# Kernel optimization log

Measured on AMD Instinct MI355X. Metric: run time of the kernel, lower is better.

Reference implementation:

```python
import jax, jax.numpy as jnp
import numpy as np

N_NODES = 50000
N_EDGES = 800000
N_ENT = 500000
N_REL = 500
L = 2          # num_layers
H = 8          # head_num
D = 16         # per-head dim (hidden_dim // head_num)
HID = H * D    # 128
IN = 128       # in_ent_dim == in_rel_dim == hidden_dim
B = 64         # number of graphs in the batch
SLOPE = 0.2    # leaky-relu negative slope


def setup_inputs() -> dict:
    key = jax.random.key(0)
    ks = jax.random.split(key, 11)
    return {
        "ent_table": jax.random.normal(ks[0], (N_ENT, IN), jnp.float32) * 0.05,
        "rel_table": jax.random.normal(ks[1], (N_REL, IN), jnp.float32) * 0.05,
        "W_ent": jax.random.normal(ks[2], (L, IN, HID), jnp.float32) * 0.05,
        "W_rel": jax.random.normal(ks[3], (L, IN, HID), jnp.float32) * 0.05,
        "attn_l": jax.random.normal(ks[4], (L, H, D), jnp.float32) * 0.05,
        "attn_r": jax.random.normal(ks[5], (L, H, D), jnp.float32) * 0.05,
        "attn_e": jax.random.normal(ks[6], (L, H, D), jnp.float32) * 0.05,
        "ent_ids": jax.random.randint(ks[7], (N_NODES,), 0, N_ENT, jnp.int32),
        "rel_ids": jax.random.randint(ks[8], (N_EDGES,), 0, N_REL, jnp.int32),
        "src": jax.random.randint(ks[9], (N_EDGES,), 0, N_NODES, jnp.int32),
        "dst": jax.random.randint(ks[10], (N_EDGES,), 0, N_NODES, jnp.int32),
        # node-0 offset of each subgraph in the batched graph
        "graph_offsets": jnp.arange(B, dtype=jnp.int32) * (N_NODES // B),
    }


def _kge_layer(h, rel_f, src, dst, W_e, W_r, a_l, a_r, a_e):
    # GAT-style relation-aware message passing (KGELayer)
    feat = (h @ W_e).reshape(-1, H, D)        # [N,H,D]
    rfeat = (rel_f @ W_r).reshape(-1, H, D)   # [E,H,D]
    el = jnp.einsum('nhd,hd->nh', feat, a_l)  # src score
    er = jnp.einsum('nhd,hd->nh', feat, a_r)  # dst score
    ee = jnp.einsum('ehd,hd->eh', rfeat, a_e) # relation score
    e = jax.nn.leaky_relu(el[src] + er[dst] + ee, SLOPE)  # [E,H]
    # segment softmax over incoming edges of each dst node
    emax = jax.ops.segment_max(e, dst, num_segments=N_NODES)
    ex = jnp.exp(e - emax[dst])
    denom = jax.ops.segment_sum(ex, dst, num_segments=N_NODES)
    alpha = ex / denom[dst]                   # [E,H]
    msg = (feat[src] + rfeat) * alpha[:, :, None]  # [E,H,D]
    out = jax.ops.segment_sum(msg, dst, num_segments=N_NODES)  # [N,H,D]
    return out.reshape(-1, HID)


def reference(ent_table, rel_table, W_ent, W_rel, attn_l, attn_r, attn_e,
              ent_ids, rel_ids, src, dst, graph_offsets):
    h = ent_table[ent_ids]       # [N,IN]
    rel_f = rel_table[rel_ids]   # [E,IN]
    for l in range(L):
        h = _kge_layer(h, rel_f, src, dst, W_ent[l], W_rel[l],
                       attn_l[l], attn_r[l], attn_e[l])
    # CLS embedding: node 0 of each unbatched subgraph
    return h[graph_offsets]      # [B,HID]
```

## Files before the change

kernel.cpp:

```cpp
#include <hip/hip_runtime.h>
#include <hip/hip_bf16.h>


#define NN   50000
#define NE   800000
#define NR   500
#define HH   8
#define DD   16
#define HIDD 128
#define BB   64

#define GRIDS 1024
#define PER   784

#define MAXE2 16384
#define MAXS1 16448
#define MAXE1 262144
#define MAXS0 50000


__global__ void k_init(int* slot2, int* slot1, int* slot0, int* counters) {
    int i = blockIdx.x * blockDim.x + threadIdx.x;
    int stride = gridDim.x * blockDim.x;
    for (int n = i; n < NN; n += stride) { slot2[n] = -1; slot1[n] = -1; slot0[n] = -1; }
    if (i < 8) counters[i] = 0;
}

__global__ void k_seed(const int* goffs, int* slot2, int* slot1, int* nodesS1) {
    int i = threadIdx.x;
    if (i < BB) {
        int n = goffs[i];
        slot2[n] = i;
        slot1[n] = -2;
        nodesS1[i] = n;
    }
}

__global__ void k_scan(const int* __restrict__ src, const int* __restrict__ dst,
                       const int* __restrict__ slotHit, int* __restrict__ slotNew,
                       int* eseg, int* ecnt, int* nseg, int* ncnt) {
    __shared__ int cE, cN;
    if (threadIdx.x == 0) { cE = 0; cN = 0; }
    __syncthreads();
    int b = blockIdx.x;
    int lo = b * PER;
    int hi = lo + PER; if (hi > NE) hi = NE;
    int* es = eseg + (size_t)b * PER;
    int* ns = nseg + (size_t)b * PER;
    for (int e = lo + threadIdx.x; e < hi; e += blockDim.x) {
        int d = dst[e];
        if (slotHit[d] >= 0) {
            int pos = atomicAdd(&cE, 1);
            es[pos] = e;
            int s = src[e];
            if (atomicCAS(&slotNew[s], -1, -2) == -1) {
                int p = atomicAdd(&cN, 1);
                ns[p] = s;
            }
        }
    }
    __syncthreads();
    if (threadIdx.x == 0) { ecnt[b] = cE; ncnt[b] = cN; }
}

__device__ int block_scan_counts(const int* cnts, int nblk, int* bases, int offset) {
    __shared__ int part[256];
    __shared__ int total_sh;
    int t = threadIdx.x;
    int per = (nblk + 255) / 256;
    int s = 0;
    for (int j = 0; j < per; j++) { int i = t * per + j; if (i < nblk) s += cnts[i]; }
    part[t] = s;
    __syncthreads();
    for (int d = 1; d < 256; d <<= 1) {
        int v = (t >= d) ? part[t - d] : 0;
        __syncthreads();
        part[t] += v;
        __syncthreads();
    }
    int run = ((t == 0) ? 0 : part[t - 1]) + offset;
    for (int j = 0; j < per; j++) {
        int i = t * per + j;
        if (i < nblk) { bases[i] = run; run += cnts[i]; }
    }
    if (t == 255) total_sh = part[255];
    __syncthreads();
    return total_sh;
}

__global__ void k_prefix2(const int* ecnt2, const int* ncnt2, int* ebase2, int* nbase2,
                          int* counters, const int* nodesS1, int* slot1, int* slot0,
                          int* nodesS0) {
    int t = threadIdx.x;
    int totE = block_scan_counts(ecnt2, GRIDS, ebase2, 0);
    int totN = block_scan_counts(ncnt2, GRIDS, nbase2, BB);
    if (t == 0) {
        counters[2] = totE;
        counters[0] = BB + totN;
        counters[1] = BB + totN;
    }
    if (t < BB) {
        int n = nodesS1[t];
        slot1[n] = t;
        slot0[n] = t;
        nodesS0[t] = n;
    }
}

__global__ void k_compact2(const int* eseg2, const int* ecnt2, const int* ebase2,
                           const int* nseg2, const int* ncnt2, const int* nbase2,
                           int* e2list, int* nodesS1, int* slot1, int* slot0,
                           int* nodesS0, int* deg2) {
    int b = blockIdx.x, t = threadIdx.x;
    int ce = ecnt2[b], cn = ncnt2[b], be = ebase2[b], bn = nbase2[b];
    const int* es = eseg2 + (size_t)b * PER;
    const int* ns = nseg2 + (size_t)b * PER;
    for (int i = t; i < ce; i += blockDim.x) {
        int g = be + i; if (g < MAXE2) e2list[g] = es[i];
    }
    for (int i = t; i < cn; i += blockDim.x) {
        int idx = bn + i;
        if (idx < MAXS1) {
            int n = ns[i];
            nodesS1[idx] = n;
            slot1[n] = idx;
            slot0[n] = idx;
            nodesS0[idx] = n;
        }
    }
    if (b == 0) { for (int i = t; i < BB; i += blockDim.x) deg2[i] = 0; }
}

__global__ void k_prefix1(const int* ecnt1, const int* ncnt1, int* ebase1, int* nbase1,
                          int* counters) {
    int t = threadIdx.x;
    int s0 = counters[1];
    int totE = block_scan_counts(ecnt1, GRIDS, ebase1, 0);
    int totN = block_scan_counts(ncnt1, GRIDS, nbase1, s0);
    if (t == 0) {
        counters[3] = totE;
        counters[1] = s0 + totN;
    }
}

__global__ void k_compact1(const int* eseg1, const int* ecnt1, const int* ebase1,
                           const int* nseg1, const int* ncnt1, const int* nbase1,
                           int* e1list, int* slot0, int* nodesS0,
                           int* deg1, const int* counters) {
    int b = blockIdx.x, t = threadIdx.x;
    int ce = ecnt1[b], cn = ncnt1[b], be = ebase1[b], bn = nbase1[b];
    const int* es = eseg1 + (size_t)b * PER;
    const int* ns = nseg1 + (size_t)b * PER;
    for (int i = t; i < ce; i += blockDim.x) {
        int g = be + i; if (g < MAXE1) e1list[g] = es[i];
    }
    for (int i = t; i < cn; i += blockDim.x) {
        int idx = bn + i;
        if (idx < MAXS0) {
            int n = ns[i];
            slot0[n] = idx;
            nodesS0[idx] = n;
        }
    }
    int cnt1 = counters[0]; if (cnt1 > MAXS1) cnt1 = MAXS1;
    for (int i = b * blockDim.x + t; i < cnt1; i += gridDim.x * blockDim.x) deg1[i] = 0;
}

__global__ void k_hist(const int* e2list, const int* e1list, const int* counters,
                       const int* dst, const int* slot2, const int* slot1,
                       int* deg2, int* deg1) {
    int i = blockIdx.x * blockDim.x + threadIdx.x;
    int stride = gridDim.x * blockDim.x;
    int c2 = counters[2]; if (c2 > MAXE2) c2 = MAXE2;
    int c1 = counters[3]; if (c1 > MAXE1) c1 = MAXE1;
    for (int k = i; k < c2; k += stride) atomicAdd(&deg2[slot2[dst[e2list[k]]]], 1);
    for (int k = i; k < c1; k += stride) atomicAdd(&deg1[slot1[dst[e1list[k]]]], 1);
}

__device__ void excl_scan_glob(const int* deg, int n, int* rp) {
    __shared__ int part[256];
    int t = threadIdx.x;
    int per = (n + 255) / 256;
    int s = 0;
    for (int j = 0; j < per; j++) { int i = t * per + j; if (i < n) s += deg[i]; }
    part[t] = s;
    __syncthreads();
    for (int d = 1; d < 256; d <<= 1) {
        int v = (t >= d) ? part[t - d] : 0;
        __syncthreads();
        part[t] += v;
        __syncthreads();
    }
    int run = (t == 0) ? 0 : part[t - 1];
    for (int j = 0; j < per; j++) {
        int i = t * per + j;
        if (i < n) { rp[i] = run; run += deg[i]; }
    }
    if (t == 255) rp[n] = part[255];
    __syncthreads();
}

__global__ void k_rowptr(const int* deg2, const int* deg1, const int* counters,
                         int* rp2, int* rp1, int* cur2, int* cur1) {
    int t = threadIdx.x;
    int cnt1 = counters[0]; if (cnt1 > MAXS1) cnt1 = MAXS1;
    excl_scan_glob(deg2, BB, rp2);
    excl_scan_glob(deg1, cnt1, rp1);
    for (int i = t; i < BB; i += blockDim.x) cur2[i] = rp2[i];
    for (int i = t; i < cnt1; i += blockDim.x) cur1[i] = rp1[i];
}

__global__ void k_scatter(const int* e2list, const int* e1list, const int* counters,
                          const int* dst, const int* slot2, const int* slot1,
                          int* cur2, int* cur1, int* csr2, int* csr1) {
    int i = blockIdx.x * blockDim.x + threadIdx.x;
    int stride = gridDim.x * blockDim.x;
    int c2 = counters[2]; if (c2 > MAXE2) c2 = MAXE2;
    int c1 = counters[3]; if (c1 > MAXE1) c1 = MAXE1;
    for (int k = i; k < c2; k += stride) {
        int e = e2list[k];
        int pos = atomicAdd(&cur2[slot2[dst[e]]], 1);
        if (pos < MAXE2) csr2[pos] = e;
    }
    for (int k = i; k < c1; k += stride) {
        int e = e1list[k];
        int pos = atomicAdd(&cur1[slot1[dst[e]]], 1);
        if (pos < MAXE1) csr1[pos] = e;
    }
}

#define FT 8
__global__ void k_relfeat0(const float* rel_table, const float* __restrict__ W_rel,
                           const float* attn_e, float* rproj, float* ee,
                           const int* nodesS0, const int* counters, const int* ent_ids,
                           const float* __restrict__ ent_table,
                           const float* __restrict__ W_ent,
                           const float* __restrict__ attn_l,
                           const float* __restrict__ attn_r,
                           float* feat0, float* el0, float* er0) {
    __shared__ float rows[FT][HIDD];
    int t = threadIdx.x;
    if (blockIdx.x < 2 * NR) {
        int l = blockIdx.x / NR, r = blockIdx.x % NR;
        rows[0][t] = rel_table[r * HIDD + t];
        __syncthreads();
        const float* W = W_rel + l * HIDD * HIDD;
        float acc = 0.f;
        for (int j = 0; j < HIDD; j++) acc += rows[0][j] * W[j * HIDD + t];
        rproj[(l * NR + r) * HIDD + t] = acc;
        rows[1][t] = acc;
        __syncthreads();
        if (t < HH) {
            float s = 0.f;
            for (int d = 0; d < DD; d++)
                s += rows[1][t * DD + d] * attn_e[(l * HH + t) * DD + d];
            ee[(l * NR + r) * HH + t] = s;
        }
        return;
    }
    int cnt = counters[1]; if (cnt > MAXS0) cnt = MAXS0;
    int tile0 = blockIdx.x - 2 * NR;
    int tstride = gridDim.x - 2 * NR;
    int nTiles = (cnt + FT - 1) / FT;
    for (int tile = tile0; tile < nTiles; tile += tstride) {
        int k0 = tile * FT;
        #pragma unroll
        for (int m = 0; m < FT; m++) {
            int k = k0 + m;
            int n = nodesS0[k < cnt ? k : 0];
            rows[m][t] = ent_table[(long)ent_ids[n] * HIDD + t];
        }
        __syncthreads();
        float acc[FT];
        #pragma unroll
        for (int m = 0; m < FT; m++) acc[m] = 0.f;
        for (int j = 0; j < HIDD; j++) {
            float w = W_ent[j * HIDD + t];
            #pragma unroll
            for (int m = 0; m < FT; m++) acc[m] += rows[m][j] * w;
        }
        __syncthreads();
        #pragma unroll
        for (int m = 0; m < FT; m++) {
            int k = k0 + m;
            if (k < cnt) feat0[k * HIDD + t] = acc[m];
            rows[m][t] = acc[m];
        }
        __syncthreads();
        {
            int m = t >> 4, idx = t & 15, h = idx >> 1, isR = idx & 1;
            int k = k0 + m;
            if (k < cnt) {
                const float* av = (isR ? attn_r : attn_l) + h * DD;
                float s = 0.f;
                for (int d = 0; d < DD; d++) s += rows[m][h * DD + d] * av[d];
                if (isR) er0[k * HH + h] = s; else el0[k * HH + h] = s;
            }
        }
        __syncthreads();
    }
}

__global__ void k_layer1(const int* counters, const int* rp1, const int* csr1,
                         const int* src, const int* rel_ids, const int* slot0,
                         const float* __restrict__ el0, const float* __restrict__ er0,
                         const float* __restrict__ ee0,
                         const float* __restrict__ feat0, const float* __restrict__ rproj0,
                         const float* __restrict__ W_ent1,
                         const float* attn_l1, const float* attn_r1,
                         float* feat1, float* el1, float* er1) {
    int cnt1 = counters[0]; if (cnt1 > MAXS1) cnt1 = MAXS1;
    int t = threadIdx.x;
    int h = t >> 4;
    __shared__ float row[HIDD];
    __shared__ float f2[HIDD];
    for (int k = blockIdx.x; k < cnt1; k += gridDim.x) {
        int lo = rp1[k], hi = rp1[k + 1];
        float er_k = er0[k * HH + h];
        float acc = 0.f, sumex = 0.f;
        for (int i = lo; i < hi; i++) {
            int e = csr1[i];
            int ks = slot0[src[e]];
            int rid = rel_ids[e];
            float sc = el0[ks * HH + h] + er_k + ee0[rid * HH + h];
            sc = sc >= 0.f ? sc : 0.2f * sc;
            float ex = __expf(sc);
            sumex += ex;
            acc += ex * (feat0[ks * HIDD + t] + rproj0[rid * HIDD + t]);
        }
        row[t] = (hi > lo) ? acc / sumex : 0.f;
        __syncthreads();
        float f = 0.f;
        for (int j = 0; j < HIDD; j++) f += row[j] * W_ent1[j * HIDD + t];
        feat1[k * HIDD + t] = f;
        f2[t] = f;
        __syncthreads();
        if (t < HH) {
            float s = 0.f;
            for (int d = 0; d < DD; d++) s += f2[t * DD + d] * attn_l1[t * DD + d];
            el1[k * HH + t] = s;
        } else if (t < 2 * HH) {
            int hh = t - HH;
            float s = 0.f;
            for (int d = 0; d < DD; d++) s += f2[hh * DD + d] * attn_r1[hh * DD + d];
            er1[k * HH + hh] = s;
        }
        __syncthreads();
    }
}

__global__ void k_layer2(const int* rp2, const int* csr2,
                         const int* src, const int* rel_ids, const int* slot1,
                         const float* __restrict__ el1, const float* __restrict__ er1,
                         const float* __restrict__ ee1,
                         const float* __restrict__ feat1, const float* __restrict__ rproj1,
                         float* out) {
    int g = blockIdx.x;
    int t = threadIdx.x;
    int h = t >> 4;
    int lo = rp2[g], hi = rp2[g + 1];
    float er_g = er1[g * HH + h];
    float acc = 0.f, sumex = 0.f;
    for (int i = lo; i < hi; i++) {
        int e = csr2[i];
        int ks = slot1[src[e]];
        int rid = rel_ids[e];
        float sc = el1[ks * HH + h] + er_g + ee1[rid * HH + h];
        sc = sc >= 0.f ? sc : 0.2f * sc;
        float ex = __expf(sc);
        sumex += ex;
        acc += ex * (feat1[ks * HIDD + t] + rproj1[rid * HIDD + t]);
    }
    out[g * HIDD + t] = (hi > lo) ? acc / sumex : 0.f;
}

extern "C" void kernel_launch(void* const* d_in, const int* in_sizes, int n_in,
                              void* d_out, int out_size, void* d_ws, size_t ws_size,
                              hipStream_t stream) {
    const float* ent_table = (const float*)d_in[0];
    const float* rel_table = (const float*)d_in[1];
    const float* W_ent     = (const float*)d_in[2];
    const float* W_rel     = (const float*)d_in[3];
    const float* attn_l    = (const float*)d_in[4];
    const float* attn_r    = (const float*)d_in[5];
    const float* attn_e    = (const float*)d_in[6];
    const int*   ent_ids   = (const int*)d_in[7];
    const int*   rel_ids   = (const int*)d_in[8];
    const int*   src       = (const int*)d_in[9];
    const int*   dst       = (const int*)d_in[10];
    const int*   goffs     = (const int*)d_in[11];
    float*       out       = (float*)d_out;

    char* p = (char*)d_ws;
    auto alloc = [&](size_t nbytes) {
        void* q = (void*)p;
        p += (nbytes + 255) & ~(size_t)255;
        return q;
    };
    float* rproj   = (float*)alloc((size_t)2 * NR * HIDD * 4);
    float* ee      = (float*)alloc((size_t)2 * NR * HH * 4);
    int*   slot2   = (int*)alloc((size_t)NN * 4);
    int*   slot1   = (int*)alloc((size_t)NN * 4);
    int*   slot0   = (int*)alloc((size_t)NN * 4);
    int*   nodesS1 = (int*)alloc((size_t)MAXS1 * 4);
    int*   nodesS0 = (int*)alloc((size_t)MAXS0 * 4);
    int*   e2list  = (int*)alloc((size_t)MAXE2 * 4);
    int*   e1list  = (int*)alloc((size_t)MAXE1 * 4);
    int*   counters= (int*)alloc(8 * 4);
    int*   eseg2   = (int*)alloc((size_t)GRIDS * PER * 4);
    int*   nseg2   = (int*)alloc((size_t)GRIDS * PER * 4);
    int*   eseg1   = (int*)alloc((size_t)GRIDS * PER * 4);
    int*   nseg1   = (int*)alloc((size_t)GRIDS * PER * 4);
    int*   ecnt2   = (int*)alloc((size_t)GRIDS * 4);
    int*   ncnt2   = (int*)alloc((size_t)GRIDS * 4);
    int*   ecnt1   = (int*)alloc((size_t)GRIDS * 4);
    int*   ncnt1   = (int*)alloc((size_t)GRIDS * 4);
    int*   ebase2  = (int*)alloc((size_t)GRIDS * 4);
    int*   nbase2  = (int*)alloc((size_t)GRIDS * 4);
    int*   ebase1  = (int*)alloc((size_t)GRIDS * 4);
    int*   nbase1  = (int*)alloc((size_t)GRIDS * 4);
    int*   deg2    = (int*)alloc((size_t)BB * 4);
    int*   rp2     = (int*)alloc((size_t)(BB + 1) * 4);
    int*   cur2    = (int*)alloc((size_t)BB * 4);
    int*   deg1    = (int*)alloc((size_t)MAXS1 * 4);
    int*   rp1     = (int*)alloc((size_t)(MAXS1 + 1) * 4);
    int*   cur1    = (int*)alloc((size_t)MAXS1 * 4);
    int*   csr2    = (int*)alloc((size_t)MAXE2 * 4);
    int*   csr1    = (int*)alloc((size_t)MAXE1 * 4);
    float* feat0   = (float*)alloc((size_t)MAXS0 * HIDD * 4);
    float* el0     = (float*)alloc((size_t)MAXS0 * HH * 4);
    float* er0     = (float*)alloc((size_t)MAXS0 * HH * 4);
    float* feat1   = (float*)alloc((size_t)MAXS1 * HIDD * 4);
    float* el1     = (float*)alloc((size_t)MAXS1 * HH * 4);
    float* er1     = (float*)alloc((size_t)MAXS1 * HH * 4);

    const float* rproj0 = rproj;
    const float* rproj1 = rproj + (size_t)NR * HIDD;
    const float* ee0 = ee;
    const float* ee1 = ee + (size_t)NR * HH;
    const float* W_ent0 = W_ent;
    const float* W_ent1 = W_ent + HIDD * HIDD;
    const float* attn_l0 = attn_l, *attn_l1 = attn_l + HH * DD;
    const float* attn_r0 = attn_r, *attn_r1 = attn_r + HH * DD;

    hipLaunchKernelGGL(k_init, dim3(256), dim3(256), 0, stream,
                       slot2, slot1, slot0, counters);
    hipLaunchKernelGGL(k_seed, dim3(1), dim3(64), 0, stream,
                       goffs, slot2, slot1, nodesS1);
    hipLaunchKernelGGL(k_scan, dim3(GRIDS), dim3(256), 0, stream,
                       src, dst, slot2, slot1, eseg2, ecnt2, nseg2, ncnt2);
    hipLaunchKernelGGL(k_prefix2, dim3(1), dim3(256), 0, stream,
                       ecnt2, ncnt2, ebase2, nbase2, counters,
                       nodesS1, slot1, slot0, nodesS0);
    hipLaunchKernelGGL(k_compact2, dim3(GRIDS), dim3(256), 0, stream,
                       eseg2, ecnt2, ebase2, nseg2, ncnt2, nbase2,
                       e2list, nodesS1, slot1, slot0, nodesS0, deg2);
    hipLaunchKernelGGL(k_scan, dim3(GRIDS), dim3(256), 0, stream,
                       src, dst, slot1, slot0, eseg1, ecnt1, nseg1, ncnt1);
    hipLaunchKernelGGL(k_prefix1, dim3(1), dim3(256), 0, stream,
                       ecnt1, ncnt1, ebase1, nbase1, counters);
    hipLaunchKernelGGL(k_compact1, dim3(GRIDS), dim3(256), 0, stream,
                       eseg1, ecnt1, ebase1, nseg1, ncnt1, nbase1,
                       e1list, slot0, nodesS0, deg1, counters);
    hipLaunchKernelGGL(k_hist, dim3(256), dim3(256), 0, stream,
                       e2list, e1list, counters, dst, slot2, slot1, deg2, deg1);
    hipLaunchKernelGGL(k_rowptr, dim3(1), dim3(256), 0, stream,
                       deg2, deg1, counters, rp2, rp1, cur2, cur1);
    hipLaunchKernelGGL(k_scatter, dim3(256), dim3(256), 0, stream,
                       e2list, e1list, counters, dst, slot2, slot1,
                       cur2, cur1, csr2, csr1);
    hipLaunchKernelGGL(k_relfeat0, dim3(2 * NR + 1024), dim3(HIDD), 0, stream,
                       rel_table, W_rel, attn_e, rproj, ee,
                       nodesS0, counters, ent_ids, ent_table, W_ent0,
                       attn_l0, attn_r0, feat0, el0, er0);
    hipLaunchKernelGGL(k_layer1, dim3(2048), dim3(HIDD), 0, stream,
                       counters, rp1, csr1, src, rel_ids, slot0,
                       el0, er0, ee0, feat0, rproj0, W_ent1,
                       attn_l1, attn_r1, feat1, el1, er1);
    hipLaunchKernelGGL(k_layer2, dim3(BB), dim3(HIDD), 0, stream,
                       rp2, csr2, src, rel_ids, slot1,
                       el1, er1, ee1, feat1, rproj1, out);
}
```

Measured before the change: 436.3 us.

## Fuse all pipeline stages into one cooperative persistent kernel with grid syncs

Measured after the change: 795.3 us. 82.3% more time.

```diff
diff --git a/kernel.cpp b/kernel.cpp
--- a/kernel.cpp
+++ b/kernel.cpp
@@ -1,5 +1,7 @@
 #include <hip/hip_runtime.h>
-#include <hip/hip_bf16.h>
+#include <hip/hip_cooperative_groups.h>
+
+namespace cg = cooperative_groups;
 
 
 #define NN   50000
@@ -10,8 +12,9 @@
 #define HIDD 128
 #define BB   64
 
-#define GRIDS 1024
-#define PER   784
+#define NBLK 256
+#define TPB  256
+#define PER  3128
 
 #define MAXE2 16384
 #define MAXS1 16448
@@ -19,53 +22,19 @@
 #define MAXS0 50000
 
 
-__global__ void k_init(int* slot2, int* slot1, int* slot0, int* counters) {
-    int i = blockIdx.x * blockDim.x + threadIdx.x;
-    int stride = gridDim.x * blockDim.x;
-    for (int n = i; n < NN; n += stride) { slot2[n] = -1; slot1[n] = -1; slot0[n] = -1; }
-    if (i < 8) counters[i] = 0;
-}
-
-__global__ void k_seed(const int* goffs, int* slot2, int* slot1, int* nodesS1) {
-    int i = threadIdx.x;
-    if (i < BB) {
-        int n = goffs[i];
-        slot2[n] = i;
-        slot1[n] = -2;
-        nodesS1[i] = n;
-    }
-}
-
-__global__ void k_scan(const int* __restrict__ src, const int* __restrict__ dst,
-                       const int* __restrict__ slotHit, int* __restrict__ slotNew,
-                       int* eseg, int* ecnt, int* nseg, int* ncnt) {
-    __shared__ int cE, cN;
-    if (threadIdx.x == 0) { cE = 0; cN = 0; }
-    __syncthreads();
-    int b = blockIdx.x;
-    int lo = b * PER;
-    int hi = lo + PER; if (hi > NE) hi = NE;
-    int* es = eseg + (size_t)b * PER;
-    int* ns = nseg + (size_t)b * PER;
-    for (int e = lo + threadIdx.x; e < hi; e += blockDim.x) {
-        int d = dst[e];
-        if (slotHit[d] >= 0) {
-            int pos = atomicAdd(&cE, 1);
-            es[pos] = e;
-            int s = src[e];
-            if (atomicCAS(&slotNew[s], -1, -2) == -1) {
-                int p = atomicAdd(&cN, 1);
-                ns[p] = s;
-            }
-        }
-    }
-    __syncthreads();
-    if (threadIdx.x == 0) { ecnt[b] = cE; ncnt[b] = cN; }
-}
-
-__device__ int block_scan_counts(const int* cnts, int nblk, int* bases, int offset) {
-    __shared__ int part[256];
-    __shared__ int total_sh;
+struct KParams {
+    const float *ent_table, *rel_table, *W_ent, *W_rel, *attn_l, *attn_r, *attn_e;
+    const int *ent_ids, *rel_ids, *src, *dst, *goffs;
+    float* out;
+    float *rproj, *ee;
+    int *slot2, *slot1, *slot0, *nodesS1, *nodesS0, *e2list, *e1list, *counters;
+    int *eseg, *nseg, *ecnt, *ncnt, *ebase, *nbase;
+    int *deg2, *rp2, *cur2, *deg1, *rp1, *cur1, *csr2, *csr1;
+    float *feat0, *el0, *er0, *feat1, *el1, *er1;
+};
+
+__device__ int block_scan_counts(const int* cnts, int nblk, int* bases, int offset,
+                                 int* part) {
     int t = threadIdx.x;
     int per = (nblk + 255) / 256;
     int s = 0;
@@ -83,102 +52,12 @@
         int i = t * per + j;
         if (i < nblk) { bases[i] = run; run += cnts[i]; }
     }
-    if (t == 255) total_sh = part[255];
+    int tot = part[255];
     __syncthreads();
-    return total_sh;
+    return tot;
 }
 
-__global__ void k_prefix2(const int* ecnt2, const int* ncnt2, int* ebase2, int* nbase2,
-                          int* counters, const int* nodesS1, int* slot1, int* slot0,
-                          int* nodesS0) {
-    int t = threadIdx.x;
-    int totE = block_scan_counts(ecnt2, GRIDS, ebase2, 0);
-    int totN = block_scan_counts(ncnt2, GRIDS, nbase2, BB);
-    if (t == 0) {
-        counters[2] = totE;
-        counters[0] = BB + totN;
-        counters[1] = BB + totN;
-    }
-    if (t < BB) {
-        int n = nodesS1[t];
-        slot1[n] = t;
-        slot0[n] = t;
-        nodesS0[t] = n;
-    }
-}
-
-__global__ void k_compact2(const int* eseg2, const int* ecnt2, const int* ebase2,
-                           const int* nseg2, const int* ncnt2, const int* nbase2,
-                           int* e2list, int* nodesS1, int* slot1, int* slot0,
-                           int* nodesS0, int* deg2) {
-    int b = blockIdx.x, t = threadIdx.x;
-    int ce = ecnt2[b], cn = ncnt2[b], be = ebase2[b], bn = nbase2[b];
-    const int* es = eseg2 + (size_t)b * PER;
-    const int* ns = nseg2 + (size_t)b * PER;
-    for (int i = t; i < ce; i += blockDim.x) {
-        int g = be + i; if (g < MAXE2) e2list[g] = es[i];
-    }
-    for (int i = t; i < cn; i += blockDim.x) {
-        int idx = bn + i;
-        if (idx < MAXS1) {
-            int n = ns[i];
-            nodesS1[idx] = n;
-            slot1[n] = idx;
-            slot0[n] = idx;
-            nodesS0[idx] = n;
-        }
-    }
-    if (b == 0) { for (int i = t; i < BB; i += blockDim.x) deg2[i] = 0; }
-}
-
-__global__ void k_prefix1(const int* ecnt1, const int* ncnt1, int* ebase1, int* nbase1,
-                          int* counters) {
-    int t = threadIdx.x;
-    int s0 = counters[1];
-    int totE = block_scan_counts(ecnt1, GRIDS, ebase1, 0);
-    int totN = block_scan_counts(ncnt1, GRIDS, nbase1, s0);
-    if (t == 0) {
-        counters[3] = totE;
-        counters[1] = s0 + totN;
-    }
-}
-
-__global__ void k_compact1(const int* eseg1, const int* ecnt1, const int* ebase1,
-                           const int* nseg1, const int* ncnt1, const int* nbase1,
-                           int* e1list, int* slot0, int* nodesS0,
-                           int* deg1, const int* counters) {
-    int b = blockIdx.x, t = threadIdx.x;
-    int ce = ecnt1[b], cn = ncnt1[b], be = ebase1[b], bn = nbase1[b];
-    const int* es = eseg1 + (size_t)b * PER;
-    const int* ns = nseg1 + (size_t)b * PER;
-    for (int i = t; i < ce; i += blockDim.x) {
-        int g = be + i; if (g < MAXE1) e1list[g] = es[i];
-    }
-    for (int i = t; i < cn; i += blockDim.x) {
-        int idx = bn + i;
-        if (idx < MAXS0) {
-            int n = ns[i];
-            slot0[n] = idx;
-            nodesS0[idx] = n;
-        }
-    }
-    int cnt1 = counters[0]; if (cnt1 > MAXS1) cnt1 = MAXS1;
-    for (int i = b * blockDim.x + t; i < cnt1; i += gridDim.x * blockDim.x) deg1[i] = 0;
-}
-
-__global__ void k_hist(const int* e2list, const int* e1list, const int* counters,
-                       const int* dst, const int* slot2, const int* slot1,
-                       int* deg2, int* deg1) {
-    int i = blockIdx.x * blockDim.x + threadIdx.x;
-    int stride = gridDim.x * blockDim.x;
-    int c2 = counters[2]; if (c2 > MAXE2) c2 = MAXE2;
-    int c1 = counters[3]; if (c1 > MAXE1) c1 = MAXE1;
-    for (int k = i; k < c2; k += stride) atomicAdd(&deg2[slot2[dst[e2list[k]]]], 1);
-    for (int k = i; k < c1; k += stride) atomicAdd(&deg1[slot1[dst[e1list[k]]]], 1);
-}
-
-__device__ void excl_scan_glob(const int* deg, int n, int* rp) {
-    __shared__ int part[256];
+__device__ void excl_scan_glob(const int* deg, int n, int* rp, int* part) {
     int t = threadIdx.x;
     int per = (n + 255) / 256;
     int s = 0;
@@ -200,196 +79,343 @@
     __syncthreads();
 }
 
-__global__ void k_rowptr(const int* deg2, const int* deg1, const int* counters,
-                         int* rp2, int* rp1, int* cur2, int* cur1) {
-    int t = threadIdx.x;
-    int cnt1 = counters[0]; if (cnt1 > MAXS1) cnt1 = MAXS1;
-    excl_scan_glob(deg2, BB, rp2);
-    excl_scan_glob(deg1, cnt1, rp1);
-    for (int i = t; i < BB; i += blockDim.x) cur2[i] = rp2[i];
-    for (int i = t; i < cnt1; i += blockDim.x) cur1[i] = rp1[i];
-}
-
-__global__ void k_scatter(const int* e2list, const int* e1list, const int* counters,
-                          const int* dst, const int* slot2, const int* slot1,
-                          int* cur2, int* cur1, int* csr2, int* csr1) {
-    int i = blockIdx.x * blockDim.x + threadIdx.x;
-    int stride = gridDim.x * blockDim.x;
-    int c2 = counters[2]; if (c2 > MAXE2) c2 = MAXE2;
-    int c1 = counters[3]; if (c1 > MAXE1) c1 = MAXE1;
-    for (int k = i; k < c2; k += stride) {
-        int e = e2list[k];
-        int pos = atomicAdd(&cur2[slot2[dst[e]]], 1);
-        if (pos < MAXE2) csr2[pos] = e;
-    }
-    for (int k = i; k < c1; k += stride) {
-        int e = e1list[k];
-        int pos = atomicAdd(&cur1[slot1[dst[e]]], 1);
-        if (pos < MAXE1) csr1[pos] = e;
-    }
-}
-
-#define FT 8
-__global__ void k_relfeat0(const float* rel_table, const float* __restrict__ W_rel,
-                           const float* attn_e, float* rproj, float* ee,
-                           const int* nodesS0, const int* counters, const int* ent_ids,
-                           const float* __restrict__ ent_table,
-                           const float* __restrict__ W_ent,
-                           const float* __restrict__ attn_l,
-                           const float* __restrict__ attn_r,
-                           float* feat0, float* el0, float* er0) {
-    __shared__ float rows[FT][HIDD];
-    int t = threadIdx.x;
-    if (blockIdx.x < 2 * NR) {
-        int l = blockIdx.x / NR, r = blockIdx.x % NR;
-        rows[0][t] = rel_table[r * HIDD + t];
-        __syncthreads();
-        const float* W = W_rel + l * HIDD * HIDD;
-        float acc = 0.f;
-        for (int j = 0; j < HIDD; j++) acc += rows[0][j] * W[j * HIDD + t];
-        rproj[(l * NR + r) * HIDD + t] = acc;
-        rows[1][t] = acc;
-        __syncthreads();
-        if (t < HH) {
-            float s = 0.f;
-            for (int d = 0; d < DD; d++)
-                s += rows[1][t * DD + d] * attn_e[(l * HH + t) * DD + d];
-            ee[(l * NR + r) * HH + t] = s;
-        }
-        return;
-    }
-    int cnt = counters[1]; if (cnt > MAXS0) cnt = MAXS0;
-    int tile0 = blockIdx.x - 2 * NR;
-    int tstride = gridDim.x - 2 * NR;
-    int nTiles = (cnt + FT - 1) / FT;
-    for (int tile = tile0; tile < nTiles; tile += tstride) {
-        int k0 = tile * FT;
-        #pragma unroll
-        for (int m = 0; m < FT; m++) {
-            int k = k0 + m;
-            int n = nodesS0[k < cnt ? k : 0];
-            rows[m][t] = ent_table[(long)ent_ids[n] * HIDD + t];
-        }
-        __syncthreads();
-        float acc[FT];
-        #pragma unroll
-        for (int m = 0; m < FT; m++) acc[m] = 0.f;
-        for (int j = 0; j < HIDD; j++) {
-            float w = W_ent[j * HIDD + t];
+__global__ void __launch_bounds__(TPB, 1) k_all(KParams P) {
+    cg::grid_group grid = cg::this_grid();
+    const int b = blockIdx.x, t = threadIdx.x;
+    const int gtid = b * TPB + t, gstride = NBLK * TPB;
+
+    __shared__ int sh_cE, sh_cN;
+    __shared__ int sh_part[256];
+    __shared__ float sh_rows[2][8][HIDD];
+
+    const float* ee0 = P.ee;
+    const float* ee1 = P.ee + NR * HH;
+    const float* rproj0 = P.rproj;
+    const float* rproj1 = P.rproj + (size_t)NR * HIDD;
+    const float* W_ent1 = P.W_ent + HIDD * HIDD;
+    const float* attn_l1 = P.attn_l + HH * DD;
+    const float* attn_r1 = P.attn_r + HH * DD;
+
+    auto scan = [&](const int* slotHit, int* slotNew) {
+        if (t == 0) { sh_cE = 0; sh_cN = 0; }
+        __syncthreads();
+        int lo = b * PER;
+        int hi = lo + PER; if (hi > NE) hi = NE;
+        int* es = P.eseg + (size_t)b * PER;
+        int* ns = P.nseg + (size_t)b * PER;
+        const int4* dst4 = (const int4*)(P.dst + lo);
+        int n4 = (hi - lo) >> 2;
+        for (int q = t; q < n4; q += TPB) {
+            int4 d4 = dst4[q];
+            int eb = lo + q * 4;
             #pragma unroll
-            for (int m = 0; m < FT; m++) acc[m] += rows[m][j] * w;
-        }
-        __syncthreads();
-        #pragma unroll
-        for (int m = 0; m < FT; m++) {
-            int k = k0 + m;
-            if (k < cnt) feat0[k * HIDD + t] = acc[m];
-            rows[m][t] = acc[m];
-        }
-        __syncthreads();
-        {
-            int m = t >> 4, idx = t & 15, h = idx >> 1, isR = idx & 1;
-            int k = k0 + m;
-            if (k < cnt) {
-                const float* av = (isR ? attn_r : attn_l) + h * DD;
+            for (int c = 0; c < 4; c++) {
+                int d = (&d4.x)[c];
+                if (slotHit[d] >= 0) {
+                    int pos = atomicAdd(&sh_cE, 1);
+                    es[pos] = eb + c;
+                    int s = P.src[eb + c];
+                    if (atomicCAS(&slotNew[s], -1, -2) == -1) {
+                        int pp = atomicAdd(&sh_cN, 1);
+                        ns[pp] = s;
+                    }
+                }
+            }
+        }
+        __syncthreads();
+        if (t == 0) { P.ecnt[b] = sh_cE; P.ncnt[b] = sh_cN; }
+    };
+
+    for (int n = gtid; n < NN; n += gstride) {
+        P.slot2[n] = -1; P.slot1[n] = -1; P.slot0[n] = -1;
+    }
+    if (gtid < 8) P.counters[gtid] = 0;
+    grid.sync();
+
+    if (b == 0 && t < BB) {
+        int n = P.goffs[t];
+        P.slot2[n] = t;
+        P.slot1[n] = -2;
+        P.nodesS1[t] = n;
+    }
+    grid.sync();
+
+    scan(P.slot2, P.slot1);
+    {
+        int sb = t >> 7, tt = t & 127;
+        int vg = NBLK * 2;
+        float (*rows)[HIDD] = sh_rows[sb];
+        int iters = (2 * NR + vg - 1) / vg;
+        for (int it = 0; it < iters; it++) {
+            int vb = b * 2 + sb + it * vg;
+            bool act = vb < 2 * NR;
+            int l = act ? vb / NR : 0, r = act ? vb % NR : 0;
+            if (act) rows[0][tt] = P.rel_table[r * HIDD + tt];
+            __syncthreads();
+            float acc = 0.f;
+            if (act) {
+                const float* W = P.W_rel + l * HIDD * HIDD;
+                for (int j = 0; j < HIDD; j++) acc += rows[0][j] * W[j * HIDD + tt];
+                P.rproj[(size_t)vb * HIDD + tt] = acc;
+            }
+            __syncthreads();
+            if (act) rows[1][tt] = acc;
+            __syncthreads();
+            if (act && tt < HH) {
                 float s = 0.f;
-                for (int d = 0; d < DD; d++) s += rows[m][h * DD + d] * av[d];
-                if (isR) er0[k * HH + h] = s; else el0[k * HH + h] = s;
-            }
-        }
-        __syncthreads();
-    }
-}
-
-__global__ void k_layer1(const int* counters, const int* rp1, const int* csr1,
-                         const int* src, const int* rel_ids, const int* slot0,
-                         const float* __restrict__ el0, const float* __restrict__ er0,
-                         const float* __restrict__ ee0,
-                         const float* __restrict__ feat0, const float* __restrict__ rproj0,
-                         const float* __restrict__ W_ent1,
-                         const float* attn_l1, const float* attn_r1,
-                         float* feat1, float* el1, float* er1) {
-    int cnt1 = counters[0]; if (cnt1 > MAXS1) cnt1 = MAXS1;
-    int t = threadIdx.x;
-    int h = t >> 4;
-    __shared__ float row[HIDD];
-    __shared__ float f2[HIDD];
-    for (int k = blockIdx.x; k < cnt1; k += gridDim.x) {
-        int lo = rp1[k], hi = rp1[k + 1];
-        float er_k = er0[k * HH + h];
-        float acc = 0.f, sumex = 0.f;
-        for (int i = lo; i < hi; i++) {
-            int e = csr1[i];
-            int ks = slot0[src[e]];
-            int rid = rel_ids[e];
-            float sc = el0[ks * HH + h] + er_k + ee0[rid * HH + h];
-            sc = sc >= 0.f ? sc : 0.2f * sc;
-            float ex = __expf(sc);
-            sumex += ex;
-            acc += ex * (feat0[ks * HIDD + t] + rproj0[rid * HIDD + t]);
-        }
-        row[t] = (hi > lo) ? acc / sumex : 0.f;
-        __syncthreads();
-        float f = 0.f;
-        for (int j = 0; j < HIDD; j++) f += row[j] * W_ent1[j * HIDD + t];
-        feat1[k * HIDD + t] = f;
-        f2[t] = f;
-        __syncthreads();
-        if (t < HH) {
-            float s = 0.f;
-            for (int d = 0; d < DD; d++) s += f2[t * DD + d] * attn_l1[t * DD + d];
-            el1[k * HH + t] = s;
-        } else if (t < 2 * HH) {
-            int hh = t - HH;
-            float s = 0.f;
-            for (int d = 0; d < DD; d++) s += f2[hh * DD + d] * attn_r1[hh * DD + d];
-            er1[k * HH + hh] = s;
-        }
-        __syncthreads();
-    }
-}
-
-__global__ void k_layer2(const int* rp2, const int* csr2,
-                         const int* src, const int* rel_ids, const int* slot1,
-                         const float* __restrict__ el1, const float* __restrict__ er1,
-                         const float* __restrict__ ee1,
-                         const float* __restrict__ feat1, const float* __restrict__ rproj1,
-                         float* out) {
-    int g = blockIdx.x;
-    int t = threadIdx.x;
-    int h = t >> 4;
-    int lo = rp2[g], hi = rp2[g + 1];
-    float er_g = er1[g * HH + h];
-    float acc = 0.f, sumex = 0.f;
-    for (int i = lo; i < hi; i++) {
-        int e = csr2[i];
-        int ks = slot1[src[e]];
-        int rid = rel_ids[e];
-        float sc = el1[ks * HH + h] + er_g + ee1[rid * HH + h];
-        sc = sc >= 0.f ? sc : 0.2f * sc;
-        float ex = __expf(sc);
-        sumex += ex;
-        acc += ex * (feat1[ks * HIDD + t] + rproj1[rid * HIDD + t]);
-    }
-    out[g * HIDD + t] = (hi > lo) ? acc / sumex : 0.f;
+                for (int d = 0; d < DD; d++)
+                    s += rows[1][tt * DD + d] * P.attn_e[(l * HH + tt) * DD + d];
+                P.ee[vb * HH + tt] = s;
+            }
+            __syncthreads();
+        }
+    }
+    grid.sync();
+
+    if (b == 0) {
+        int totE = block_scan_counts(P.ecnt, NBLK, P.ebase, 0, sh_part);
+        int totN = block_scan_counts(P.ncnt, NBLK, P.nbase, BB, sh_part);
+        if (t == 0) {
+            P.counters[2] = min(totE, MAXE2);
+            int s1 = min(BB + totN, MAXS1);
+            P.counters[0] = s1;
+            P.counters[1] = s1;
+        }
+        if (t < BB) {
+            int n = P.nodesS1[t];
+            P.slot1[n] = t;
+            P.slot0[n] = t;
+            P.nodesS0[t] = n;
+        }
+    }
+    grid.sync();
+
+    {
+        int ce = P.ecnt[b], cn = P.ncnt[b], be = P.ebase[b], bn = P.nbase[b];
+        const int* es = P.eseg + (size_t)b * PER;
+        const int* ns = P.nseg + (size_t)b * PER;
+        for (int i = t; i < ce; i += TPB) {
+            int g = be + i; if (g < MAXE2) P.e2list[g] = es[i];
+        }
+        for (int i = t; i < cn; i += TPB) {
+            int idx = bn + i;
+            if (idx < MAXS1) {
+                int n = ns[i];
+                P.nodesS1[idx] = n;
+                P.slot1[n] = idx;
+                P.slot0[n] = idx;
+                P.nodesS0[idx] = n;
+            }
+        }
+        if (b == 0) for (int i = t; i < BB; i += TPB) P.deg2[i] = 0;
+    }
+    grid.sync();
+
+    scan(P.slot1, P.slot0);
+    grid.sync();
+
+    if (b == 0) {
+        int s0 = P.counters[1];
+        int totE = block_scan_counts(P.ecnt, NBLK, P.ebase, 0, sh_part);
+        int totN = block_scan_counts(P.ncnt, NBLK, P.nbase, s0, sh_part);
+        if (t == 0) {
+            P.counters[3] = min(totE, MAXE1);
+            P.counters[1] = min(s0 + totN, MAXS0);
+        }
+    }
+    grid.sync();
+
+    {
+        int ce = P.ecnt[b], cn = P.ncnt[b], be = P.ebase[b], bn = P.nbase[b];
+        const int* es = P.eseg + (size_t)b * PER;
+        const int* ns = P.nseg + (size_t)b * PER;
+        for (int i = t; i < ce; i += TPB) {
+            int g = be + i; if (g < MAXE1) P.e1list[g] = es[i];
+        }
+        for (int i = t; i < cn; i += TPB) {
+            int idx = bn + i;
+            if (idx < MAXS0) {
+                int n = ns[i];
+                P.slot0[n] = idx;
+                P.nodesS0[idx] = n;
+            }
+        }
+        int cnt1 = P.counters[0];
+        for (int i = gtid; i < cnt1; i += gstride) P.deg1[i] = 0;
+    }
+    grid.sync();
+
+    {
+        int c2 = P.counters[2], c1 = P.counters[3];
+        for (int k = gtid; k < c2; k += gstride)
+            atomicAdd(&P.deg2[P.slot2[P.dst[P.e2list[k]]]], 1);
+        for (int k = gtid; k < c1; k += gstride)
+            atomicAdd(&P.deg1[P.slot1[P.dst[P.e1list[k]]]], 1);
+    }
+    {
+        int cnt = P.counters[1];
+        int sb = t >> 7, tt = t & 127;
+        int vg = NBLK * 2;
+        float (*rows)[HIDD] = sh_rows[sb];
+        int nT = (cnt + 7) / 8;
+        int iters = (nT + vg - 1) / vg;
+        for (int it = 0; it < iters; it++) {
+            int tile = b * 2 + sb + it * vg;
+            bool act = tile < nT;
+            int k0 = tile * 8;
+            #pragma unroll
+            for (int m = 0; m < 8; m++) {
+                int k = k0 + m;
+                int n = P.nodesS0[(act && k < cnt) ? k : 0];
+                rows[m][tt] = P.ent_table[(size_t)P.ent_ids[n] * HIDD + tt];
+            }
+            __syncthreads();
+            float acc[8];
+            #pragma unroll
+            for (int m = 0; m < 8; m++) acc[m] = 0.f;
+            if (act) {
+                for (int j = 0; j < HIDD; j++) {
+                    float w = P.W_ent[j * HIDD + tt];
+                    #pragma unroll
+                    for (int m = 0; m < 8; m++) acc[m] += rows[m][j] * w;
+                }
+            }
+            __syncthreads();
+            #pragma unroll
+            for (int m = 0; m < 8; m++) {
+                int k = k0 + m;
+                if (act && k < cnt) P.feat0[(size_t)k * HIDD + tt] = acc[m];
+                rows[m][tt] = acc[m];
+            }
+            __syncthreads();
+            {
+                int m = tt >> 4, idx = tt & 15, h = idx >> 1, isR = idx & 1;
+                int k = k0 + m;
+                if (act && k < cnt) {
+                    const float* av = (isR ? P.attn_r : P.attn_l) + h * DD;
+                    float s = 0.f;
+                    for (int d = 0; d < DD; d++) s += rows[m][h * DD + d] * av[d];
+                    if (isR) P.er0[k * HH + h] = s; else P.el0[k * HH + h] = s;
+                }
+            }
+            __syncthreads();
+        }
+    }
+    grid.sync();
+
+    if (b == 0) {
+        int cnt1 = P.counters[0];
+        excl_scan_glob(P.deg2, BB, P.rp2, sh_part);
+        excl_scan_glob(P.deg1, cnt1, P.rp1, sh_part);
+        for (int i = t; i < BB; i += TPB) P.cur2[i] = P.rp2[i];
+        for (int i = t; i < cnt1; i += TPB) P.cur1[i] = P.rp1[i];
+    }
+    grid.sync();
+
+    {
+        int c2 = P.counters[2], c1 = P.counters[3];
+        for (int k = gtid; k < c2; k += gstride) {
+            int e = P.e2list[k];
+            int pos = atomicAdd(&P.cur2[P.slot2[P.dst[e]]], 1);
+            if (pos < MAXE2) P.csr2[pos] = e;
+        }
+        for (int k = gtid; k < c1; k += gstride) {
+            int e = P.e1list[k];
+            int pos = atomicAdd(&P.cur1[P.slot1[P.dst[e]]], 1);
+            if (pos < MAXE1) P.csr1[pos] = e;
+        }
+    }
+    grid.sync();
+
+    {
+        int cnt1 = P.counters[0];
+        int sb = t >> 7, tt = t & 127, h = tt >> 4;
+        int vg = NBLK * 2;
+        float* row = (float*)sh_rows[sb];
+        float* f2  = ((float*)sh_rows[sb]) + HIDD;
+        int iters = (cnt1 + vg - 1) / vg;
+        for (int it = 0; it < iters; it++) {
+            int k = b * 2 + sb + it * vg;
+            bool act = k < cnt1;
+            int lo = 0, hi = 0;
+            float er_k = 0.f;
+            if (act) { lo = P.rp1[k]; hi = P.rp1[k + 1]; er_k = P.er0[k * HH + h]; }
+            float accv = 0.f, sumex = 0.f;
+            for (int i = lo; i < hi; i++) {
+                int e = P.csr1[i];
+                int ks = P.slot0[P.src[e]];
+                int rid = P.rel_ids[e];
+                float sc = P.el0[ks * HH + h] + er_k + ee0[rid * HH + h];
+                sc = sc >= 0.f ? sc : 0.2f * sc;
+                float ex = __expf(sc);
+                sumex += ex;
+                accv += ex * (P.feat0[(size_t)ks * HIDD + tt] + rproj0[rid * HIDD + tt]);
+            }
+            if (act) row[tt] = (hi > lo) ? accv / sumex : 0.f;
+            __syncthreads();
+            float f = 0.f;
+            if (act) {
+                for (int j = 0; j < HIDD; j++) f += row[j] * W_ent1[j * HIDD + tt];
+                P.feat1[(size_t)k * HIDD + tt] = f;
+                f2[tt] = f;
+            }
+            __syncthreads();
+            if (act) {
+                if (tt < HH) {
+                    float s = 0.f;
+                    for (int d = 0; d < DD; d++) s += f2[tt * DD + d] * attn_l1[tt * DD + d];
+                    P.el1[k * HH + tt] = s;
+                } else if (tt < 2 * HH) {
+                    int hh = tt - HH;
+                    float s = 0.f;
+                    for (int d = 0; d < DD; d++) s += f2[hh * DD + d] * attn_r1[hh * DD + d];
+                    P.er1[k * HH + hh] = s;
+                }
+            }
+            __syncthreads();
+        }
+    }
+    grid.sync();
+
+    {
+        int sb = t >> 7, tt = t & 127, h = tt >> 4;
+        int vb = b * 2 + sb;
+        if (vb < BB) {
+            int lo = P.rp2[vb], hi = P.rp2[vb + 1];
+            float er_g = P.er1[vb * HH + h];
+            float accv = 0.f, sumex = 0.f;
+            for (int i = lo; i < hi; i++) {
+                int e = P.csr2[i];
+                int ks = P.slot1[P.src[e]];
+                int rid = P.rel_ids[e];
+                float sc = P.el1[ks * HH + h] + er_g + ee1[rid * HH + h];
+                sc = sc >= 0.f ? sc : 0.2f * sc;
+                float ex = __expf(sc);
+                sumex += ex;
+                accv += ex * (P.feat1[(size_t)ks * HIDD + tt] + rproj1[rid * HIDD + tt]);
+            }
+            P.out[vb * HIDD + tt] = (hi > lo) ? accv / sumex : 0.f;
+        }
+    }
 }
 
 extern "C" void kernel_launch(void* const* d_in, const int* in_sizes, int n_in,
                               void* d_out, int out_size, void* d_ws, size_t ws_size,
                               hipStream_t stream) {
-    const float* ent_table = (const float*)d_in[0];
-    const float* rel_table = (const float*)d_in[1];
-    const float* W_ent     = (const float*)d_in[2];
-    const float* W_rel     = (const float*)d_in[3];
-    const float* attn_l    = (const float*)d_in[4];
-    const float* attn_r    = (const float*)d_in[5];
-    const float* attn_e    = (const float*)d_in[6];
-    const int*   ent_ids   = (const int*)d_in[7];
-    const int*   rel_ids   = (const int*)d_in[8];
-    const int*   src       = (const int*)d_in[9];
-    const int*   dst       = (const int*)d_in[10];
-    const int*   goffs     = (const int*)d_in[11];
-    float*       out       = (float*)d_out;
+    KParams prm;
+    prm.ent_table = (const float*)d_in[0];
+    prm.rel_table = (const float*)d_in[1];
+    prm.W_ent     = (const float*)d_in[2];
+    prm.W_rel     = (const float*)d_in[3];
+    prm.attn_l    = (const float*)d_in[4];
+    prm.attn_r    = (const float*)d_in[5];
+    prm.attn_e    = (const float*)d_in[6];
+    prm.ent_ids   = (const int*)d_in[7];
+    prm.rel_ids   = (const int*)d_in[8];
+    prm.src       = (const int*)d_in[9];
+    prm.dst       = (const int*)d_in[10];
+    prm.goffs     = (const int*)d_in[11];
+    prm.out       = (float*)d_out;
 
     char* p = (char*)d_ws;
     auto alloc = [&](size_t nbytes) {
@@ -397,87 +423,38 @@
         p += (nbytes + 255) & ~(size_t)255;
         return q;
     };
-    float* rproj   = (float*)alloc((size_t)2 * NR * HIDD * 4);
-    float* ee      = (float*)alloc((size_t)2 * NR * HH * 4);
-    int*   slot2   = (int*)alloc((size_t)NN * 4);
-    int*   slot1   = (int*)alloc((size_t)NN * 4);
-    int*   slot0   = (int*)alloc((size_t)NN * 4);
-    int*   nodesS1 = (int*)alloc((size_t)MAXS1 * 4);
-    int*   nodesS0 = (int*)alloc((size_t)MAXS0 * 4);
-    int*   e2list  = (int*)alloc((size_t)MAXE2 * 4);
-    int*   e1list  = (int*)alloc((size_t)MAXE1 * 4);
-    int*   counters= (int*)alloc(8 * 4);
-    int*   eseg2   = (int*)alloc((size_t)GRIDS * PER * 4);
-    int*   nseg2   = (int*)alloc((size_t)GRIDS * PER * 4);
-    int*   eseg1   = (int*)alloc((size_t)GRIDS * PER * 4);
-    int*   nseg1   = (int*)alloc((size_t)GRIDS * PER * 4);
-    int*   ecnt2   = (int*)alloc((size_t)GRIDS * 4);
-    int*   ncnt2   = (int*)alloc((size_t)GRIDS * 4);
-    int*   ecnt1   = (int*)alloc((size_t)GRIDS * 4);
-    int*   ncnt1   = (int*)alloc((size_t)GRIDS * 4);
-    int*   ebase2  = (int*)alloc((size_t)GRIDS * 4);
-    int*   nbase2  = (int*)alloc((size_t)GRIDS * 4);
-    int*   ebase1  = (int*)alloc((size_t)GRIDS * 4);
-    int*   nbase1  = (int*)alloc((size_t)GRIDS * 4);
-    int*   deg2    = (int*)alloc((size_t)BB * 4);
-    int*   rp2     = (int*)alloc((size_t)(BB + 1) * 4);
-    int*   cur2    = (int*)alloc((size_t)BB * 4);
-    int*   deg1    = (int*)alloc((size_t)MAXS1 * 4);
-    int*   rp1     = (int*)alloc((size_t)(MAXS1 + 1) * 4);
-    int*   cur1    = (int*)alloc((size_t)MAXS1 * 4);
-    int*   csr2    = (int*)alloc((size_t)MAXE2 * 4);
-    int*   csr1    = (int*)alloc((size_t)MAXE1 * 4);
-    float* feat0   = (float*)alloc((size_t)MAXS0 * HIDD * 4);
-    float* el0     = (float*)alloc((size_t)MAXS0 * HH * 4);
-    float* er0     = (float*)alloc((size_t)MAXS0 * HH * 4);
-    float* feat1   = (float*)alloc((size_t)MAXS1 * HIDD * 4);
-    float* el1     = (float*)alloc((size_t)MAXS1 * HH * 4);
-    float* er1     = (float*)alloc((size_t)MAXS1 * HH * 4);
-
-    const float* rproj0 = rproj;
-    const float* rproj1 = rproj + (size_t)NR * HIDD;
-    const float* ee0 = ee;
-    const float* ee1 = ee + (size_t)NR * HH;
-    const float* W_ent0 = W_ent;
-    const float* W_ent1 = W_ent + HIDD * HIDD;
-    const float* attn_l0 = attn_l, *attn_l1 = attn_l + HH * DD;
-    const float* attn_r0 = attn_r, *attn_r1 = attn_r + HH * DD;
-
-    hipLaunchKernelGGL(k_init, dim3(256), dim3(256), 0, stream,
-                       slot2, slot1, slot0, counters);
-    hipLaunchKernelGGL(k_seed, dim3(1), dim3(64), 0, stream,
-                       goffs, slot2, slot1, nodesS1);
-    hipLaunchKernelGGL(k_scan, dim3(GRIDS), dim3(256), 0, stream,
-                       src, dst, slot2, slot1, eseg2, ecnt2, nseg2, ncnt2);
-    hipLaunchKernelGGL(k_prefix2, dim3(1), dim3(256), 0, stream,
-                       ecnt2, ncnt2, ebase2, nbase2, counters,
-                       nodesS1, slot1, slot0, nodesS0);
-    hipLaunchKernelGGL(k_compact2, dim3(GRIDS), dim3(256), 0, stream,
-                       eseg2, ecnt2, ebase2, nseg2, ncnt2, nbase2,
-                       e2list, nodesS1, slot1, slot0, nodesS0, deg2);
-    hipLaunchKernelGGL(k_scan, dim3(GRIDS), dim3(256), 0, stream,
-                       src, dst, slot1, slot0, eseg1, ecnt1, nseg1, ncnt1);
-    hipLaunchKernelGGL(k_prefix1, dim3(1), dim3(256), 0, stream,
-                       ecnt1, ncnt1, ebase1, nbase1, counters);
-    hipLaunchKernelGGL(k_compact1, dim3(GRIDS), dim3(256), 0, stream,
-                       eseg1, ecnt1, ebase1, nseg1, ncnt1, nbase1,
-                       e1list, slot0, nodesS0, deg1, counters);
-    hipLaunchKernelGGL(k_hist, dim3(256), dim3(256), 0, stream,
-                       e2list, e1list, counters, dst, slot2, slot1, deg2, deg1);
-    hipLaunchKernelGGL(k_rowptr, dim3(1), dim3(256), 0, stream,
-                       deg2, deg1, counters, rp2, rp1, cur2, cur1);
-    hipLaunchKernelGGL(k_scatter, dim3(256), dim3(256), 0, stream,
-                       e2list, e1list, counters, dst, slot2, slot1,
-                       cur2, cur1, csr2, csr1);
-    hipLaunchKernelGGL(k_relfeat0, dim3(2 * NR + 1024), dim3(HIDD), 0, stream,
-                       rel_table, W_rel, attn_e, rproj, ee,
-                       nodesS0, counters, ent_ids, ent_table, W_ent0,
-                       attn_l0, attn_r0, feat0, el0, er0);
-    hipLaunchKernelGGL(k_layer1, dim3(2048), dim3(HIDD), 0, stream,
-                       counters, rp1, csr1, src, rel_ids, slot0,
-                       el0, er0, ee0, feat0, rproj0, W_ent1,
-                       attn_l1, attn_r1, feat1, el1, er1);
-    hipLaunchKernelGGL(k_layer2, dim3(BB), dim3(HIDD), 0, stream,
-                       rp2, csr2, src, rel_ids, slot1,
-                       el1, er1, ee1, feat1, rproj1, out);
+    prm.rproj   = (float*)alloc((size_t)2 * NR * HIDD * 4);
+    prm.ee      = (float*)alloc((size_t)2 * NR * HH * 4);
+    prm.slot2   = (int*)alloc((size_t)NN * 4);
+    prm.slot1   = (int*)alloc((size_t)NN * 4);
+    prm.slot0   = (int*)alloc((size_t)NN * 4);
+    prm.nodesS1 = (int*)alloc((size_t)MAXS1 * 4);
+    prm.nodesS0 = (int*)alloc((size_t)MAXS0 * 4);
+    prm.e2list  = (int*)alloc((size_t)MAXE2 * 4);
+    prm.e1list  = (int*)alloc((size_t)MAXE1 * 4);
+    prm.counters= (int*)alloc(8 * 4);
+    prm.eseg    = (int*)alloc((size_t)NBLK * PER * 4);
+    prm.nseg    = (int*)alloc((size_t)NBLK * PER * 4);
+    prm.ecnt    = (int*)alloc((size_t)NBLK * 4);
+    prm.ncnt    = (int*)alloc((size_t)NBLK * 4);
+    prm.ebase   = (int*)alloc((size_t)NBLK * 4);
+    prm.nbase   = (int*)alloc((size_t)NBLK * 4);
+    prm.deg2    = (int*)alloc((size_t)BB * 4);
+    prm.rp2     = (int*)alloc((size_t)(BB + 1) * 4);
+    prm.cur2    = (int*)alloc((size_t)BB * 4);
+    prm.deg1    = (int*)alloc((size_t)MAXS1 * 4);
+    prm.rp1     = (int*)alloc((size_t)(MAXS1 + 1) * 4);
+    prm.cur1    = (int*)alloc((size_t)MAXS1 * 4);
+    prm.csr2    = (int*)alloc((size_t)MAXE2 * 4);
+    prm.csr1    = (int*)alloc((size_t)MAXE1 * 4);
+    prm.feat0   = (float*)alloc((size_t)MAXS0 * HIDD * 4);
+    prm.el0     = (float*)alloc((size_t)MAXS0 * HH * 4);
+    prm.er0     = (float*)alloc((size_t)MAXS0 * HH * 4);
+    prm.feat1   = (float*)alloc((size_t)MAXS1 * HIDD * 4);
+    prm.el1     = (float*)alloc((size_t)MAXS1 * HH * 4);
+    prm.er1     = (float*)alloc((size_t)MAXS1 * HH * 4);
+
+    void* args[] = { (void*)&prm };
+    hipLaunchCooperativeKernel(reinterpret_cast<void*>(k_all),
+                               dim3(NBLK), dim3(TPB), args, 0, stream);
 }
```
